# Performance work log

Measured on AMD Instinct MI355X. Metric: run time of the kernel, lower is better.

## Reference

```python
import jax, jax.numpy as jnp
import numpy as np

V, D, B, NEG = 100000, 128, 4096, 5
D_INNER = int(D * 2.0 * 2 / 3)  # nGPT FF inner dim = 170

def l2norm(t, axis=-1):
    return t / jnp.linalg.norm(t, axis=axis, keepdims=True)

def setup_inputs() -> dict:
    key = jax.random.key(0)
    ks = jax.random.split(key, 8)
    return {
        "input_ids": jax.random.randint(ks[0], (B,), 0, V),
        "target_ids": jax.random.randint(ks[1], (B,), 0, V),
        "neg_ids": jax.random.randint(ks[2], (B, NEG), 0, V),
        "W_in": jax.random.normal(ks[3], (V, D), jnp.float32) * (1.0 / np.sqrt(D)),
        "W_out": jax.random.normal(ks[4], (V, D), jnp.float32) * (1.0 / np.sqrt(D)),
        "W_hidden": jax.random.normal(ks[5], (D_INNER, D), jnp.float32) * 0.02,
        "W_gate": jax.random.normal(ks[6], (D_INNER, D), jnp.float32) * 0.02,
        "W_ff_out": jax.random.normal(ks[7], (D, D_INNER), jnp.float32) * 0.02,
        "hidden_scale": jnp.ones((D_INNER,), jnp.float32),
        "gate_scale": jnp.ones((D_INNER,), jnp.float32),
        "logit_scale": jnp.full((V,), D ** -0.5, dtype=jnp.float32),  # Scale param init = s_logit_scale
    }

def reference(input_ids, target_ids, neg_ids, W_in, W_out, W_hidden, W_gate,
              W_ff_out, hidden_scale, gate_scale, logit_scale):
    # skipgram: gather normalized input embeddings
    emb = l2norm(W_in)[input_ids]                                  # (B, D)
    # nGPT FeedForward: silu-gated, weights l2-normalized on input dim
    h = (emb @ l2norm(W_hidden).T) * hidden_scale                  # (B, D_INNER)
    g = (emb @ l2norm(W_gate).T) * gate_scale * jnp.sqrt(jnp.float32(D))
    x = jax.nn.silu(g) * h
    x = x @ l2norm(W_ff_out, axis=0).T                             # (B, D), to_out norm_dim_in=False
    # logits over full vocab, scaled by Scale(): param * (init/scale)
    scale_eff = logit_scale * (1.0 / (D ** -0.5))                  # (V,)
    logits = (x @ l2norm(W_out).T) * scale_eff                     # (B, V)
    # negative-sampling loss: gather positive + sampled negative logits
    pos = jnp.take_along_axis(logits, target_ids[:, None], axis=1)  # (B, 1)
    neg = jnp.take_along_axis(logits, neg_ids, axis=1)              # (B, NEG)
    positive_loss = jax.nn.log_sigmoid(pos).mean()
    negative_loss = jax.nn.log_sigmoid(-neg).mean()
    return -(positive_loss + negative_loss)
```

## Files before the change

### kernel.cpp

```cpp
#include <hip/hip_runtime.h>
#include <math.h>

#define DD   128
#define DI   170
#define BB   4096
#define NNEG 5
#define ROWS 8
#define NBLK (BB / ROWS)
#define TASKS (ROWS * (1 + NNEG))
#define TPW  (TASKS / 4)
#define SQRT_D 11.3137084989847603904f

__device__ __forceinline__ float wave_bcast_sum(float v) {
#pragma unroll
    for (int m = 1; m < 64; m <<= 1) v += __shfl_xor(v, m, 64);
    return v;
}

__global__ __launch_bounds__(256) void norms_kernel(
    const float* __restrict__ W_hidden,
    const float* __restrict__ W_gate,
    const float* __restrict__ W_ff_out,
    float* __restrict__ inv_h,
    float* __restrict__ inv_g,
    float* __restrict__ inv_f,
    float* __restrict__ out)
{
    if (blockIdx.x == 0 && threadIdx.x == 0) out[0] = 0.0f;
    if (blockIdx.x < 85) {
        const int wave = threadIdx.x >> 6;
        const int lane = threadIdx.x & 63;
        const int v = blockIdx.x * 4 + wave;
        const float* W = (v < DI) ? W_hidden : W_gate;
        const int row = (v < DI) ? v : v - DI;
        float2 p = ((const float2*)(W + (long)row * DD))[lane];
        float s = wave_bcast_sum(p.x * p.x + p.y * p.y);
        if (lane == 0) {
            float inv = rsqrtf(s);
            if (v < DI) inv_h[v] = inv; else inv_g[v - DI] = inv;
        }
    } else {
        const int c = threadIdx.x;
        if (c < DI) {
            float s = 0.0f;
#pragma unroll 4
            for (int d = 0; d < DD; ++d) {
                float a = W_ff_out[(long)d * DI + c];
                s += a * a;
            }
            inv_f[c] = rsqrtf(s);
        }
    }
}

__global__ __launch_bounds__(256) void main_kernel(
    const int*   __restrict__ input_ids,
    const int*   __restrict__ target_ids,
    const int*   __restrict__ neg_ids,
    const float* __restrict__ W_in,
    const float* __restrict__ W_out,
    const float* __restrict__ W_hidden,
    const float* __restrict__ W_gate,
    const float* __restrict__ W_ff_out,
    const float* __restrict__ hidden_scale,
    const float* __restrict__ gate_scale,
    const float* __restrict__ logit_scale,
    const float* __restrict__ inv_h,
    const float* __restrict__ inv_g,
    const float* __restrict__ inv_f,
    float* __restrict__ out)
{
    __shared__ float s_emb[ROWS][DD];
    __shared__ float s_x[ROWS][DI + 2];
    __shared__ float s_xout[ROWS][DD];
    __shared__ float s_red[4];

    const int tid  = threadIdx.x;
    const int wave = tid >> 6;
    const int lane = tid & 63;
    const int b0   = blockIdx.x * ROWS;

#pragma unroll
    for (int k = 0; k < ROWS / 4; ++k) {
        const int r  = wave + 4 * k;
        const int id = input_ids[b0 + r];
        float2 p = ((const float2*)(W_in + (long)id * DD))[lane];
        float s  = wave_bcast_sum(p.x * p.x + p.y * p.y);
        float inv = rsqrtf(s);
        s_emb[r][2 * lane]     = p.x * inv;
        s_emb[r][2 * lane + 1] = p.y * inv;
    }
    __syncthreads();

    if (tid < DI) {
        const int i = tid;
        float ah[ROWS], ag[ROWS];
#pragma unroll
        for (int r = 0; r < ROWS; ++r) { ah[r] = 0.0f; ag[r] = 0.0f; }
        const float4* wh = (const float4*)(W_hidden + (long)i * DD);
        const float4* wg = (const float4*)(W_gate   + (long)i * DD);
#pragma unroll 4
        for (int d4 = 0; d4 < DD / 4; ++d4) {
            float4 h4 = wh[d4];
            float4 g4 = wg[d4];
#pragma unroll
            for (int r = 0; r < ROWS; ++r) {
                float4 e4 = ((const float4*)s_emb[r])[d4];
                ah[r] += e4.x * h4.x + e4.y * h4.y + e4.z * h4.z + e4.w * h4.w;
                ag[r] += e4.x * g4.x + e4.y * g4.y + e4.z * g4.z + e4.w * g4.w;
            }
        }
        const float hs = hidden_scale[i] * inv_h[i];
        const float gs = gate_scale[i]   * inv_g[i] * SQRT_D;
        const float fi = inv_f[i];
#pragma unroll
        for (int r = 0; r < ROWS; ++r) {
            float h = ah[r] * hs;
            float g = ag[r] * gs;
            float x = (g / (1.0f + __expf(-g))) * h;
            s_x[r][i] = x * fi;
        }
    }
    __syncthreads();

    {
        const int dd = tid & 127;
        const int r0 = tid >> 7;
        float acc[ROWS / 2];
#pragma unroll
        for (int k = 0; k < ROWS / 2; ++k) acc[k] = 0.0f;
        const float2* wrow = (const float2*)(W_ff_out + (long)dd * DI);
#pragma unroll 5
        for (int i2 = 0; i2 < DI / 2; ++i2) {
            float2 wf = wrow[i2];
#pragma unroll
            for (int k = 0; k < ROWS / 2; ++k) {
                const int r = r0 + 2 * k;
                float2 xv = *(const float2*)&s_x[r][2 * i2];
                acc[k] += xv.x * wf.x + xv.y * wf.y;
            }
        }
#pragma unroll
        for (int k = 0; k < ROWS / 2; ++k) s_xout[r0 + 2 * k][dd] = acc[k];
    }
    __syncthreads();

    float dotp[TPW], ssp[TPW], lsc[TPW];
    const int tbase = wave * TPW;
#pragma unroll
    for (int k = 0; k < TPW; ++k) {
        const int t  = tbase + k;
        const int r  = t / (1 + NNEG);
        const int jj = t % (1 + NNEG);
        const int bidx = b0 + r;
        const int id = (jj == 0) ? target_ids[bidx] : neg_ids[bidx * NNEG + jj - 1];
        const float* wrow = W_out + (long)id * DD;
        float w0 = wrow[lane], w1 = wrow[64 + lane];
        float x0 = s_xout[r][lane], x1 = s_xout[r][64 + lane];
        dotp[k] = w0 * x0 + w1 * x1;
        ssp[k]  = w0 * w0 + w1 * w1;
        lsc[k]  = logit_scale[id];
    }
    float wacc = 0.0f;
#pragma unroll
    for (int k = 0; k < TPW; ++k) {
        float dot = dotp[k], ss = ssp[k];
#pragma unroll
        for (int m = 1; m < 64; m <<= 1) {
            dot += __shfl_xor(dot, m, 64);
            ss  += __shfl_xor(ss,  m, 64);
        }
        const int jj = (tbase + k) % (1 + NNEG);
        const float logit = dot * rsqrtf(ss) * lsc[k] * SQRT_D;
        const float z  = (jj == 0) ? logit : -logit;
        const float ls = fminf(z, 0.0f) - log1pf(__expf(-fabsf(z)));
        wacc += (jj == 0) ? ls * (1.0f / BB) : ls * (1.0f / (BB * NNEG));
    }
    if (lane == 0) s_red[wave] = wacc;
    __syncthreads();
    if (tid == 0) {
        float tot = s_red[0] + s_red[1] + s_red[2] + s_red[3];
        atomicAdd(out, -tot);
    }
}

extern "C" void kernel_launch(void* const* d_in, const int* in_sizes, int n_in,
                              void* d_out, int out_size, void* d_ws, size_t ws_size,
                              hipStream_t stream) {
    (void)in_sizes; (void)n_in; (void)out_size; (void)ws_size;
    const int*   input_ids    = (const int*)  d_in[0];
    const int*   target_ids   = (const int*)  d_in[1];
    const int*   neg_ids      = (const int*)  d_in[2];
    const float* W_in         = (const float*)d_in[3];
    const float* W_out        = (const float*)d_in[4];
    const float* W_hidden     = (const float*)d_in[5];
    const float* W_gate       = (const float*)d_in[6];
    const float* W_ff_out     = (const float*)d_in[7];
    const float* hidden_scale = (const float*)d_in[8];
    const float* gate_scale   = (const float*)d_in[9];
    const float* logit_scale  = (const float*)d_in[10];
    float* out   = (float*)d_out;
    float* inv_h = (float*)d_ws;
    float* inv_g = inv_h + DI;
    float* inv_f = inv_g + DI;

    norms_kernel<<<86, 256, 0, stream>>>(W_hidden, W_gate, W_ff_out,
                                         inv_h, inv_g, inv_f, out);
    main_kernel<<<NBLK, 256, 0, stream>>>(input_ids, target_ids, neg_ids,
                                          W_in, W_out, W_hidden, W_gate, W_ff_out,
                                          hidden_scale, gate_scale, logit_scale,
                                          inv_h, inv_g, inv_f, out);
}
```

Baseline: 174.0 us.

## Transpose FF weights in prep kernel for coalesced loads in main kernel

The prep kernel now also writes transposed, float4-interleaved copies of W_hidden, W_gate and a zero-padded transposed W_ff_out into workspace. The main kernel reads these so that adjacent threads load adjacent float4s, replacing per-thread strided row reads that were uncoalesced. The second matmul now uses float4 vectors over a zero-padded inner dimension. The cost is extra prep work and workspace traffic, plus a prep grid of 108 blocks.

```diff
diff --git a/kernel.cpp b/kernel.cpp
--- a/kernel.cpp
+++ b/kernel.cpp
@@ -3,6 +3,7 @@
 
 #define DD   128
 #define DI   170
+#define DIP4 43
 #define BB   4096
 #define NNEG 5
 #define ROWS 8
@@ -17,29 +18,35 @@
     return v;
 }
 
-__global__ __launch_bounds__(256) void norms_kernel(
+__global__ __launch_bounds__(256) void prep_kernel(
     const float* __restrict__ W_hidden,
     const float* __restrict__ W_gate,
     const float* __restrict__ W_ff_out,
+    float* __restrict__ whT,
+    float* __restrict__ wgT,
+    float* __restrict__ wfT,
     float* __restrict__ inv_h,
     float* __restrict__ inv_g,
     float* __restrict__ inv_f,
     float* __restrict__ out)
 {
-    if (blockIdx.x == 0 && threadIdx.x == 0) out[0] = 0.0f;
-    if (blockIdx.x < 85) {
+    const int blk = blockIdx.x;
+    if (blk < 85) {
         const int wave = threadIdx.x >> 6;
         const int lane = threadIdx.x & 63;
-        const int v = blockIdx.x * 4 + wave;
+        const int v = blk * 4 + wave;
         const float* W = (v < DI) ? W_hidden : W_gate;
-        const int row = (v < DI) ? v : v - DI;
+        float*       T = (v < DI) ? whT : wgT;
+        const int  row = (v < DI) ? v : v - DI;
         float2 p = ((const float2*)(W + (long)row * DD))[lane];
+        ((float2*)(T + (((lane >> 1) * DI + row) << 2)))[lane & 1] = p;
         float s = wave_bcast_sum(p.x * p.x + p.y * p.y);
         if (lane == 0) {
             float inv = rsqrtf(s);
-            if (v < DI) inv_h[v] = inv; else inv_g[v - DI] = inv;
-        }
-    } else {
+            if (v < DI) inv_h[row] = inv; else inv_g[row] = inv;
+        }
+    } else if (blk == 85) {
+        if (threadIdx.x == 0) out[0] = 0.0f;
         const int c = threadIdx.x;
         if (c < DI) {
             float s = 0.0f;
@@ -50,6 +57,20 @@
             }
             inv_f[c] = rsqrtf(s);
         }
+    } else {
+        const int t = (blk - 86) * 256 + threadIdx.x;
+        if (t < DIP4 * DD) {
+            const int dd = t / DIP4;
+            const int i4 = t - dd * DIP4;
+            const float* src = W_ff_out + (long)dd * DI;
+            float4 v4;
+            const int i = 4 * i4;
+            v4.x = (i + 0 < DI) ? src[i + 0] : 0.0f;
+            v4.y = (i + 1 < DI) ? src[i + 1] : 0.0f;
+            v4.z = (i + 2 < DI) ? src[i + 2] : 0.0f;
+            v4.w = (i + 3 < DI) ? src[i + 3] : 0.0f;
+            ((float4*)wfT)[i4 * DD + dd] = v4;
+        }
     }
 }
 
@@ -59,9 +80,9 @@
     const int*   __restrict__ neg_ids,
     const float* __restrict__ W_in,
     const float* __restrict__ W_out,
-    const float* __restrict__ W_hidden,
-    const float* __restrict__ W_gate,
-    const float* __restrict__ W_ff_out,
+    const float* __restrict__ whT,
+    const float* __restrict__ wgT,
+    const float* __restrict__ wfT,
     const float* __restrict__ hidden_scale,
     const float* __restrict__ gate_scale,
     const float* __restrict__ logit_scale,
@@ -70,9 +91,9 @@
     const float* __restrict__ inv_f,
     float* __restrict__ out)
 {
-    __shared__ float s_emb[ROWS][DD];
-    __shared__ float s_x[ROWS][DI + 2];
-    __shared__ float s_xout[ROWS][DD];
+    __shared__ __align__(16) float s_emb[ROWS][DD];
+    __shared__ __align__(16) float s_x[ROWS][4 * DIP4];
+    __shared__ __align__(16) float s_xout[ROWS][DD];
     __shared__ float s_red[4];
 
     const int tid  = threadIdx.x;
@@ -97,12 +118,12 @@
         float ah[ROWS], ag[ROWS];
 #pragma unroll
         for (int r = 0; r < ROWS; ++r) { ah[r] = 0.0f; ag[r] = 0.0f; }
-        const float4* wh = (const float4*)(W_hidden + (long)i * DD);
-        const float4* wg = (const float4*)(W_gate   + (long)i * DD);
+        const float4* wh4 = (const float4*)whT;
+        const float4* wg4 = (const float4*)wgT;
 #pragma unroll 4
         for (int d4 = 0; d4 < DD / 4; ++d4) {
-            float4 h4 = wh[d4];
-            float4 g4 = wg[d4];
+            float4 h4 = wh4[d4 * DI + i];
+            float4 g4 = wg4[d4 * DI + i];
 #pragma unroll
             for (int r = 0; r < ROWS; ++r) {
                 float4 e4 = ((const float4*)s_emb[r])[d4];
@@ -120,6 +141,9 @@
             float x = (g / (1.0f + __expf(-g))) * h;
             s_x[r][i] = x * fi;
         }
+    } else if (tid < 4 * DIP4) {
+#pragma unroll
+        for (int r = 0; r < ROWS; ++r) s_x[r][tid] = 0.0f;
     }
     __syncthreads();
 
@@ -129,15 +153,15 @@
         float acc[ROWS / 2];
 #pragma unroll
         for (int k = 0; k < ROWS / 2; ++k) acc[k] = 0.0f;
-        const float2* wrow = (const float2*)(W_ff_out + (long)dd * DI);
-#pragma unroll 5
-        for (int i2 = 0; i2 < DI / 2; ++i2) {
-            float2 wf = wrow[i2];
+        const float4* wf4 = (const float4*)wfT;
+#pragma unroll 4
+        for (int i4 = 0; i4 < DIP4; ++i4) {
+            float4 wf = wf4[i4 * DD + dd];
 #pragma unroll
             for (int k = 0; k < ROWS / 2; ++k) {
                 const int r = r0 + 2 * k;
-                float2 xv = *(const float2*)&s_x[r][2 * i2];
-                acc[k] += xv.x * wf.x + xv.y * wf.y;
+                float4 xv = *(const float4*)&s_x[r][4 * i4];
+                acc[k] += xv.x * wf.x + xv.y * wf.y + xv.z * wf.z + xv.w * wf.w;
             }
         }
 #pragma unroll
@@ -199,15 +223,20 @@
     const float* hidden_scale = (const float*)d_in[8];
     const float* gate_scale   = (const float*)d_in[9];
     const float* logit_scale  = (const float*)d_in[10];
-    float* out   = (float*)d_out;
-    float* inv_h = (float*)d_ws;
+    float* out = (float*)d_out;
+
+    float* whT   = (float*)d_ws;
+    float* wgT   = whT + 21760;
+    float* wfT   = wgT + 21760;
+    float* inv_h = wfT + 22016;
     float* inv_g = inv_h + DI;
     float* inv_f = inv_g + DI;
 
-    norms_kernel<<<86, 256, 0, stream>>>(W_hidden, W_gate, W_ff_out,
+    prep_kernel<<<108, 256, 0, stream>>>(W_hidden, W_gate, W_ff_out,
+                                         whT, wgT, wfT,
                                          inv_h, inv_g, inv_f, out);
     main_kernel<<<NBLK, 256, 0, stream>>>(input_ids, target_ids, neg_ids,
-                                          W_in, W_out, W_hidden, W_gate, W_ff_out,
+                                          W_in, W_out, whT, wgT, wfT,
                                           hidden_scale, gate_scale, logit_scale,
                                           inv_h, inv_g, inv_f, out);
 }
```

After: 174.2 us. About the same (+0.1%).

## Spread FF hidden/gate matvec across all 256 threads and pad shared rows

Applied to the files above, without the earlier changes.

The hidden/gate projection now uses all 256 threads. Each thread handles one batch row and six inner indices, instead of only 170 threads each doing all 8 rows. The shared-memory pitches are padded to 132 and 172 floats to reduce bank conflicts, and the ff_out stage reassigns threads so neighbouring lanes share a W_ff_out row. The aim is to raise thread utilisation in the FF stage. In exchange, each thread issues more uncoalesced global weight loads across 6 rows, and the last index is clamped and its store masked.

```diff
diff --git a/kernel.cpp b/kernel.cpp
--- a/kernel.cpp
+++ b/kernel.cpp
@@ -10,6 +10,8 @@
 #define TASKS (ROWS * (1 + NNEG))
 #define TPW  (TASKS / 4)
 #define SQRT_D 11.3137084989847603904f
+#define EMB_PITCH 132
+#define X_PITCH   172
 
 __device__ __forceinline__ float wave_bcast_sum(float v) {
 #pragma unroll
@@ -26,7 +28,6 @@
     float* __restrict__ inv_f,
     float* __restrict__ out)
 {
-    if (blockIdx.x == 0 && threadIdx.x == 0) out[0] = 0.0f;
     if (blockIdx.x < 85) {
         const int wave = threadIdx.x >> 6;
         const int lane = threadIdx.x & 63;
@@ -37,9 +38,10 @@
         float s = wave_bcast_sum(p.x * p.x + p.y * p.y);
         if (lane == 0) {
             float inv = rsqrtf(s);
-            if (v < DI) inv_h[v] = inv; else inv_g[v - DI] = inv;
+            if (v < DI) inv_h[row] = inv; else inv_g[row] = inv;
         }
     } else {
+        if (threadIdx.x == 0) out[0] = 0.0f;
         const int c = threadIdx.x;
         if (c < DI) {
             float s = 0.0f;
@@ -70,9 +72,9 @@
     const float* __restrict__ inv_f,
     float* __restrict__ out)
 {
-    __shared__ float s_emb[ROWS][DD];
-    __shared__ float s_x[ROWS][DI + 2];
-    __shared__ float s_xout[ROWS][DD];
+    __shared__ __align__(16) float s_emb[ROWS][EMB_PITCH];
+    __shared__ __align__(16) float s_x[ROWS][X_PITCH];
+    __shared__ __align__(16) float s_xout[ROWS][DD];
     __shared__ float s_red[4];
 
     const int tid  = threadIdx.x;
@@ -92,56 +94,60 @@
     }
     __syncthreads();
 
-    if (tid < DI) {
-        const int i = tid;
-        float ah[ROWS], ag[ROWS];
-#pragma unroll
-        for (int r = 0; r < ROWS; ++r) { ah[r] = 0.0f; ag[r] = 0.0f; }
-        const float4* wh = (const float4*)(W_hidden + (long)i * DD);
-        const float4* wg = (const float4*)(W_gate   + (long)i * DD);
-#pragma unroll 4
+    {
+        const int r  = tid & 7;
+        const int ig = tid >> 3;
+        int idx[6];
+#pragma unroll
+        for (int k = 0; k < 6; ++k) idx[k] = ig + 32 * k;
+        if (idx[5] > DI - 1) idx[5] = DI - 1;
+
+        float ah[6], ag[6];
+#pragma unroll
+        for (int k = 0; k < 6; ++k) { ah[k] = 0.0f; ag[k] = 0.0f; }
+
         for (int d4 = 0; d4 < DD / 4; ++d4) {
-            float4 h4 = wh[d4];
-            float4 g4 = wg[d4];
-#pragma unroll
-            for (int r = 0; r < ROWS; ++r) {
-                float4 e4 = ((const float4*)s_emb[r])[d4];
-                ah[r] += e4.x * h4.x + e4.y * h4.y + e4.z * h4.z + e4.w * h4.w;
-                ag[r] += e4.x * g4.x + e4.y * g4.y + e4.z * g4.z + e4.w * g4.w;
+            float4 e4 = *(const float4*)&s_emb[r][4 * d4];
+#pragma unroll
+            for (int k = 0; k < 6; ++k) {
+                float4 h4 = *(const float4*)(W_hidden + (long)idx[k] * DD + 4 * d4);
+                float4 g4 = *(const float4*)(W_gate   + (long)idx[k] * DD + 4 * d4);
+                ah[k] += e4.x * h4.x + e4.y * h4.y + e4.z * h4.z + e4.w * h4.w;
+                ag[k] += e4.x * g4.x + e4.y * g4.y + e4.z * g4.z + e4.w * g4.w;
             }
         }
-        const float hs = hidden_scale[i] * inv_h[i];
-        const float gs = gate_scale[i]   * inv_g[i] * SQRT_D;
-        const float fi = inv_f[i];
-#pragma unroll
-        for (int r = 0; r < ROWS; ++r) {
-            float h = ah[r] * hs;
-            float g = ag[r] * gs;
-            float x = (g / (1.0f + __expf(-g))) * h;
-            s_x[r][i] = x * fi;
+#pragma unroll
+        for (int k = 0; k < 6; ++k) {
+            const int i = idx[k];
+            const float hs = hidden_scale[i] * inv_h[i];
+            const float gs = gate_scale[i]   * inv_g[i] * SQRT_D;
+            const float h = ah[k] * hs;
+            const float g = ag[k] * gs;
+            const float x = (g / (1.0f + __expf(-g))) * h;
+            if (k < 5 || ig < DI - 160)
+                s_x[r][i] = x * inv_f[i];
         }
     }
     __syncthreads();
 
     {
-        const int dd = tid & 127;
-        const int r0 = tid >> 7;
-        float acc[ROWS / 2];
-#pragma unroll
-        for (int k = 0; k < ROWS / 2; ++k) acc[k] = 0.0f;
+        const int dd = tid >> 1;
+        const int rq = tid & 1;
+        float acc[4];
+#pragma unroll
+        for (int j = 0; j < 4; ++j) acc[j] = 0.0f;
         const float2* wrow = (const float2*)(W_ff_out + (long)dd * DI);
 #pragma unroll 5
         for (int i2 = 0; i2 < DI / 2; ++i2) {
             float2 wf = wrow[i2];
 #pragma unroll
-            for (int k = 0; k < ROWS / 2; ++k) {
-                const int r = r0 + 2 * k;
-                float2 xv = *(const float2*)&s_x[r][2 * i2];
-                acc[k] += xv.x * wf.x + xv.y * wf.y;
+            for (int j = 0; j < 4; ++j) {
+                float2 xv = *(const float2*)&s_x[rq * 4 + j][2 * i2];
+                acc[j] += xv.x * wf.x + xv.y * wf.y;
             }
         }
 #pragma unroll
-        for (int k = 0; k < ROWS / 2; ++k) s_xout[r0 + 2 * k][dd] = acc[k];
+        for (int j = 0; j < 4; ++j) s_xout[rq * 4 + j][dd] = acc[j];
     }
     __syncthreads();
 
```

Result: slower. 179.7 us (+3.3%).

## Split fused main kernel into separate FFN and output-logit kernels

Applied to the files above, without the earlier changes.

Splits the single fused kernel into two. An FFN kernel tiles 16 batch rows by 64 inner columns, so every thread in the block does useful work, and writes the gated activations to a global workspace. An output kernel reloads those activations, applies the output projection and computes the sampled-logit loss. Each FFN block now reads only a slice of the hidden and gate weights, which cuts repeated L2 weight traffic and idle threads. The cost is an extra kernel launch plus a round trip of the intermediate buffer through global memory.

```diff
diff --git a/kernel.cpp b/kernel.cpp
--- a/kernel.cpp
+++ b/kernel.cpp
@@ -5,11 +5,20 @@
 #define DI   170
 #define BB   4096
 #define NNEG 5
-#define ROWS 8
-#define NBLK (BB / ROWS)
-#define TASKS (ROWS * (1 + NNEG))
-#define TPW  (TASKS / 4)
 #define SQRT_D 11.3137084989847603904f
+
+#define EMB_PITCH 132
+#define XPITCH    172
+#define X4        43
+
+#define R2ROWS 16
+#define NROWT  (BB / R2ROWS)
+#define NFFN   (NROWT * 3)
+
+#define R3ROWS 8
+#define NOUT   (BB / R3ROWS)
+#define TASKS  (R3ROWS * (1 + NNEG))
+#define TPW    (TASKS / 4)
 
 __device__ __forceinline__ float wave_bcast_sum(float v) {
 #pragma unroll
@@ -26,7 +35,6 @@
     float* __restrict__ inv_f,
     float* __restrict__ out)
 {
-    if (blockIdx.x == 0 && threadIdx.x == 0) out[0] = 0.0f;
     if (blockIdx.x < 85) {
         const int wave = threadIdx.x >> 6;
         const int lane = threadIdx.x & 63;
@@ -37,9 +45,10 @@
         float s = wave_bcast_sum(p.x * p.x + p.y * p.y);
         if (lane == 0) {
             float inv = rsqrtf(s);
-            if (v < DI) inv_h[v] = inv; else inv_g[v - DI] = inv;
+            if (v < DI) inv_h[row] = inv; else inv_g[row] = inv;
         }
     } else {
+        if (threadIdx.x == 0) out[0] = 0.0f;
         const int c = threadIdx.x;
         if (c < DI) {
             float s = 0.0f;
@@ -53,95 +62,118 @@
     }
 }
 
-__global__ __launch_bounds__(256) void main_kernel(
+__global__ __launch_bounds__(256) void ffn_kernel(
     const int*   __restrict__ input_ids,
-    const int*   __restrict__ target_ids,
-    const int*   __restrict__ neg_ids,
     const float* __restrict__ W_in,
-    const float* __restrict__ W_out,
     const float* __restrict__ W_hidden,
     const float* __restrict__ W_gate,
-    const float* __restrict__ W_ff_out,
     const float* __restrict__ hidden_scale,
     const float* __restrict__ gate_scale,
-    const float* __restrict__ logit_scale,
     const float* __restrict__ inv_h,
     const float* __restrict__ inv_g,
     const float* __restrict__ inv_f,
-    float* __restrict__ out)
+    float* __restrict__ X)
 {
-    __shared__ float s_emb[ROWS][DD];
-    __shared__ float s_x[ROWS][DI + 2];
-    __shared__ float s_xout[ROWS][DD];
-    __shared__ float s_red[4];
+    __shared__ __align__(16) float s_emb[R2ROWS][EMB_PITCH];
 
     const int tid  = threadIdx.x;
     const int wave = tid >> 6;
     const int lane = tid & 63;
-    const int b0   = blockIdx.x * ROWS;
-
-#pragma unroll
-    for (int k = 0; k < ROWS / 4; ++k) {
-        const int r  = wave + 4 * k;
-        const int id = input_ids[b0 + r];
-        float2 p = ((const float2*)(W_in + (long)id * DD))[lane];
-        float s  = wave_bcast_sum(p.x * p.x + p.y * p.y);
+    const int bt = blockIdx.x;
+    const int it = bt % 3;
+    const int rt = bt / 3;
+    const int b0 = rt * R2ROWS;
+    const int i0 = it * 64;
+    const int wi = (it == 2) ? (DI - 128) : 64;
+
+    int ids[4];
+#pragma unroll
+    for (int k = 0; k < 4; ++k) ids[k] = input_ids[b0 + wave * 4 + k];
+    float2 p[4];
+#pragma unroll
+    for (int k = 0; k < 4; ++k)
+        p[k] = ((const float2*)(W_in + (long)ids[k] * DD))[lane];
+#pragma unroll
+    for (int k = 0; k < 4; ++k) {
+        float s = wave_bcast_sum(p[k].x * p[k].x + p[k].y * p[k].y);
         float inv = rsqrtf(s);
-        s_emb[r][2 * lane]     = p.x * inv;
-        s_emb[r][2 * lane + 1] = p.y * inv;
-    }
-    __syncthreads();
-
-    if (tid < DI) {
-        const int i = tid;
-        float ah[ROWS], ag[ROWS];
-#pragma unroll
-        for (int r = 0; r < ROWS; ++r) { ah[r] = 0.0f; ag[r] = 0.0f; }
-        const float4* wh = (const float4*)(W_hidden + (long)i * DD);
-        const float4* wg = (const float4*)(W_gate   + (long)i * DD);
+        s_emb[wave * 4 + k][2 * lane]     = p[k].x * inv;
+        s_emb[wave * 4 + k][2 * lane + 1] = p[k].y * inv;
+    }
+    __syncthreads();
+
+    const bool act = lane < wi;
+    const int i = i0 + (act ? lane : wi - 1);
+    float ah[4] = {0.f, 0.f, 0.f, 0.f};
+    float ag[4] = {0.f, 0.f, 0.f, 0.f};
+    const float4* wh = (const float4*)(W_hidden + (long)i * DD);
+    const float4* wg = (const float4*)(W_gate   + (long)i * DD);
 #pragma unroll 4
-        for (int d4 = 0; d4 < DD / 4; ++d4) {
-            float4 h4 = wh[d4];
-            float4 g4 = wg[d4];
-#pragma unroll
-            for (int r = 0; r < ROWS; ++r) {
-                float4 e4 = ((const float4*)s_emb[r])[d4];
-                ah[r] += e4.x * h4.x + e4.y * h4.y + e4.z * h4.z + e4.w * h4.w;
-                ag[r] += e4.x * g4.x + e4.y * g4.y + e4.z * g4.z + e4.w * g4.w;
-            }
-        }
-        const float hs = hidden_scale[i] * inv_h[i];
-        const float gs = gate_scale[i]   * inv_g[i] * SQRT_D;
-        const float fi = inv_f[i];
-#pragma unroll
-        for (int r = 0; r < ROWS; ++r) {
-            float h = ah[r] * hs;
-            float g = ag[r] * gs;
-            float x = (g / (1.0f + __expf(-g))) * h;
-            s_x[r][i] = x * fi;
-        }
+    for (int d4 = 0; d4 < DD / 4; ++d4) {
+        float4 h4 = wh[d4];
+        float4 g4 = wg[d4];
+#pragma unroll
+        for (int j = 0; j < 4; ++j) {
+            float4 e4 = *(const float4*)&s_emb[wave * 4 + j][4 * d4];
+            ah[j] += e4.x * h4.x + e4.y * h4.y + e4.z * h4.z + e4.w * h4.w;
+            ag[j] += e4.x * g4.x + e4.y * g4.y + e4.z * g4.z + e4.w * g4.w;
+        }
+    }
+    const float hs = hidden_scale[i] * inv_h[i];
+    const float gs = gate_scale[i]   * inv_g[i] * SQRT_D;
+    const float fi = inv_f[i];
+    if (act) {
+#pragma unroll
+        for (int j = 0; j < 4; ++j) {
+            const float h = ah[j] * hs;
+            const float g = ag[j] * gs;
+            const float x = (g / (1.0f + __expf(-g))) * h;
+            X[(long)(b0 + wave * 4 + j) * XPITCH + i] = x * fi;
+        }
+    }
+}
+
+__global__ __launch_bounds__(256) void out_kernel(
+    const int*   __restrict__ target_ids,
+    const int*   __restrict__ neg_ids,
+    const float* __restrict__ W_out,
+    const float* __restrict__ W_ff_out,
+    const float* __restrict__ logit_scale,
+    const float* __restrict__ X,
+    float* __restrict__ out)
+{
+    __shared__ __align__(16) float s_x[R3ROWS][XPITCH];
+    __shared__ __align__(16) float s_xout[R3ROWS][DD];
+    __shared__ float s_red[4];
+
+    const int tid  = threadIdx.x;
+    const int wave = tid >> 6;
+    const int lane = tid & 63;
+    const int b0   = blockIdx.x * R3ROWS;
+
+#pragma unroll
+    for (int idx = tid; idx < R3ROWS * X4; idx += 256) {
+        const int r = idx / X4, c = idx - r * X4;
+        ((float4*)&s_x[r][0])[c] = ((const float4*)(X + (long)(b0 + r) * XPITCH))[c];
     }
     __syncthreads();
 
     {
         const int dd = tid & 127;
         const int r0 = tid >> 7;
-        float acc[ROWS / 2];
-#pragma unroll
-        for (int k = 0; k < ROWS / 2; ++k) acc[k] = 0.0f;
+        float acc[4] = {0.f, 0.f, 0.f, 0.f};
         const float2* wrow = (const float2*)(W_ff_out + (long)dd * DI);
 #pragma unroll 5
         for (int i2 = 0; i2 < DI / 2; ++i2) {
             float2 wf = wrow[i2];
 #pragma unroll
-            for (int k = 0; k < ROWS / 2; ++k) {
-                const int r = r0 + 2 * k;
-                float2 xv = *(const float2*)&s_x[r][2 * i2];
+            for (int k = 0; k < 4; ++k) {
+                float2 xv = *(const float2*)&s_x[r0 + 2 * k][2 * i2];
                 acc[k] += xv.x * wf.x + xv.y * wf.y;
             }
         }
 #pragma unroll
-        for (int k = 0; k < ROWS / 2; ++k) s_xout[r0 + 2 * k][dd] = acc[k];
+        for (int k = 0; k < 4; ++k) s_xout[r0 + 2 * k][dd] = acc[k];
     }
     __syncthreads();
 
@@ -199,15 +231,18 @@
     const float* hidden_scale = (const float*)d_in[8];
     const float* gate_scale   = (const float*)d_in[9];
     const float* logit_scale  = (const float*)d_in[10];
-    float* out   = (float*)d_out;
-    float* inv_h = (float*)d_ws;
+    float* out = (float*)d_out;
+
+    float* X     = (float*)d_ws;
+    float* inv_h = X + (long)BB * XPITCH;
     float* inv_g = inv_h + DI;
     float* inv_f = inv_g + DI;
 
     norms_kernel<<<86, 256, 0, stream>>>(W_hidden, W_gate, W_ff_out,
                                          inv_h, inv_g, inv_f, out);
-    main_kernel<<<NBLK, 256, 0, stream>>>(input_ids, target_ids, neg_ids,
-                                          W_in, W_out, W_hidden, W_gate, W_ff_out,
-                                          hidden_scale, gate_scale, logit_scale,
-                                          inv_h, inv_g, inv_f, out);
-}
+    ffn_kernel<<<NFFN, 256, 0, stream>>>(input_ids, W_in, W_hidden, W_gate,
+                                         hidden_scale, gate_scale,
+                                         inv_h, inv_g, inv_f, X);
+    out_kernel<<<NOUT, 256, 0, stream>>>(target_ids, neg_ids, W_out, W_ff_out,
+                                         logit_scale, X, out);
+}
```

Result: slower. 182.9 us (+5.1%).
